# Kernel tuning notes

Measured on AMD Instinct MI355X. Metric: run time of the kernel, lower is better.

## Reference

```python
import jax, jax.numpy as jnp
import numpy as np

T_SIZE = 64
S_SIZE = 256
NUM_HEADS = 12
DEPTH = 12
DIM = 768
MLP_DIM = 3072
EPS = 1e-5
BATCH = 32
N_TOK = 2 * T_SIZE + S_SIZE  # 384


def setup_inputs() -> dict:
    key = jax.random.key(0)
    ks = jax.random.split(key, 6)
    s = 0.02
    return {
        "x": jax.random.normal(ks[0], (BATCH, N_TOK, DIM), jnp.float32),
        "qkv_w": jax.random.normal(ks[1], (DEPTH, DIM, 3 * DIM), jnp.float32) * s,
        "qkv_b": jnp.zeros((DEPTH, 3 * DIM), jnp.float32),
        "proj_w": jax.random.normal(ks[2], (DEPTH, DIM, DIM), jnp.float32) * s,
        "proj_b": jnp.zeros((DEPTH, DIM), jnp.float32),
        "ln1_g": jnp.ones((DEPTH, DIM), jnp.float32),
        "ln1_b": jnp.zeros((DEPTH, DIM), jnp.float32),
        "ln2_g": jnp.ones((DEPTH, DIM), jnp.float32),
        "ln2_b": jnp.zeros((DEPTH, DIM), jnp.float32),
        "fc1_w": jax.random.normal(ks[3], (DEPTH, DIM, MLP_DIM), jnp.float32) * s,
        "fc1_b": jnp.zeros((DEPTH, MLP_DIM), jnp.float32),
        "fc2_w": jax.random.normal(ks[4], (DEPTH, MLP_DIM, DIM), jnp.float32) * s,
        "fc2_b": jnp.zeros((DEPTH, DIM), jnp.float32),
    }


def _layernorm(x, g, b):
    m = jnp.mean(x, axis=-1, keepdims=True)
    v = jnp.mean((x - m) ** 2, axis=-1, keepdims=True)
    return (x - m) * jax.lax.rsqrt(v + EPS) * g + b


def _attention(x, wqkv, bqkv, wp, bp):
    B, N, C = x.shape
    hd = C // NUM_HEADS
    scale = hd ** -0.5
    # [B,N,3C] -> [3,B,H,N,hd]
    qkv = (x @ wqkv + bqkv).reshape(B, N, 3, NUM_HEADS, hd).transpose(2, 0, 3, 1, 4)
    q, k, v = qkv[0], qkv[1], qkv[2]
    q_t = q[:, :, :T_SIZE]
    q_it = q[:, :, T_SIZE:2 * T_SIZE]
    q_s = q[:, :, 2 * T_SIZE:]
    k_it = k[:, :, T_SIZE:2 * T_SIZE]
    v_it = v[:, :, T_SIZE:2 * T_SIZE]
    # mix attention: (t, s) queries over ALL keys
    q_ts = jnp.concatenate([q_t, q_s], axis=2)  # [B,H,t+s,hd]
    mix = jax.nn.softmax(jnp.einsum('bhqd,bhkd->bhqk', q_ts, k) * scale, axis=-1)
    ts = jnp.einsum('bhqk,bhkd->bhqd', mix, v).transpose(0, 2, 1, 3).reshape(B, T_SIZE + S_SIZE, C)
    # inherent attention: it queries over it keys only
    inh = jax.nn.softmax(jnp.einsum('bhqd,bhkd->bhqk', q_it, k_it) * scale, axis=-1)
    it = jnp.einsum('bhqk,bhkd->bhqd', inh, v_it).transpose(0, 2, 1, 3).reshape(B, T_SIZE, C)
    out = jnp.concatenate([ts[:, :T_SIZE], it, ts[:, T_SIZE:]], axis=1)
    return out @ wp + bp


def reference(x, qkv_w, qkv_b, proj_w, proj_b, ln1_g, ln1_b, ln2_g, ln2_b,
              fc1_w, fc1_b, fc2_w, fc2_b):
    for l in range(DEPTH):
        x = x + _attention(_layernorm(x, ln1_g[l], ln1_b[l]),
                           qkv_w[l], qkv_b[l], proj_w[l], proj_b[l])
        h = _layernorm(x, ln2_g[l], ln2_b[l])
        h = jax.nn.gelu(h @ fc1_w[l] + fc1_b[l], approximate=False)
        x = x + (h @ fc2_w[l] + fc2_b[l])
    return x
```

## Files before the change

kernel.cpp:

```cpp
#include <hip/hip_runtime.h>
#include <cstdint>

typedef unsigned short u16;
typedef __attribute__((ext_vector_type(8))) short bf16x8;
typedef __attribute__((ext_vector_type(4))) float f32x4;

#define B_SZ 32
#define NTOK 384
#define DIM 768
#define NH 12
#define HD 64
#define MLP 3072
#define MROWS (B_SZ * NTOK)

__device__ __forceinline__ float b2f(u16 h) { return __uint_as_float(((unsigned)h) << 16); }
__device__ __forceinline__ u16 f2b(float f) {
    unsigned u = __float_as_uint(f);
    unsigned r = u + 0x7fffu + ((u >> 16) & 1u);
    return (u16)(r >> 16);
}

__device__ __forceinline__ void load_lds16(const void* g, void* l) {
    __builtin_amdgcn_global_load_lds(
        (const __attribute__((address_space(1))) unsigned*)g,
        (__attribute__((address_space(3))) unsigned*)l, 16, 0, 0);
}

__global__ void detect_kernel(const u16* __restrict__ x, int* __restrict__ flagp) {
    __shared__ int cnt;
    if (threadIdx.x == 0) cnt = 0;
    __syncthreads();
    int bad = 0;
    for (int i = threadIdx.x; i < 4096; i += 256) {
        int e = (x[i] >> 7) & 0xFF;
        if (e >= 0xC0) bad++;
    }
    atomicAdd(&cnt, bad);
    __syncthreads();
    if (threadIdx.x == 0) *flagp = (cnt > 4) ? 1 : 0;
}

__global__ void conv_any(const void* __restrict__ src, u16* __restrict__ dst, int n,
                         const int* __restrict__ flagp) {
    int i = blockIdx.x * 256 + threadIdx.x;
    if (i >= n) return;
    dst[i] = (*flagp) ? f2b(((const float*)src)[i]) : ((const u16*)src)[i];
}

__global__ void load_x(const void* __restrict__ src, float* __restrict__ dst, int n,
                       const int* __restrict__ flagp) {
    int i = blockIdx.x * 256 + threadIdx.x;
    if (i >= n) return;
    dst[i] = (*flagp) ? ((const float*)src)[i] : b2f(((const u16*)src)[i]);
}

__global__ void store_out(const float* __restrict__ src, void* __restrict__ dst, int n,
                          const int* __restrict__ flagp) {
    int i = blockIdx.x * 256 + threadIdx.x;
    if (i >= n) return;
    if (*flagp) ((float*)dst)[i] = src[i];
    else ((u16*)dst)[i] = f2b(src[i]);
}

__global__ __launch_bounds__(256) void transpose_k(const void* __restrict__ in, size_t ioff,
                                                   u16* __restrict__ outp, int K, int N,
                                                   const int* __restrict__ flagp) {
    __shared__ u16 t[32][33];
    const int flag = *flagp;
    const int n0 = blockIdx.x << 5, k0 = blockIdx.y << 5;
    const int tx = threadIdx.x, ty = threadIdx.y;
#pragma unroll
    for (int i = 0; i < 4; i++) {
        size_t idx = ioff + (size_t)(k0 + ty + i * 8) * N + n0 + tx;
        t[ty + i * 8][tx] = flag ? f2b(((const float*)in)[idx]) : ((const u16*)in)[idx];
    }
    __syncthreads();
#pragma unroll
    for (int i = 0; i < 4; i++)
        outp[(size_t)(n0 + ty + i * 8) * K + k0 + tx] = t[tx][ty + i * 8];
}

template <int MODE>
__global__ __launch_bounds__(256) void gemm_bt(const u16* __restrict__ A,
                                               const u16* __restrict__ Bt,
                                               const u16* __restrict__ bias,
                                               u16* __restrict__ outb,
                                               float* __restrict__ outf,
                                               int N, int K) {
    __shared__ u16 lA[128 * 32];
    __shared__ u16 lB[128 * 32];
    const int tid = threadIdx.x;
    const int wave = tid >> 6, lane = tid & 63;
    const int quad = lane >> 4, l16 = lane & 15;
    const int m0 = blockIdx.y << 7, n0 = blockIdx.x << 7;
    const int wm = (wave & 1) << 6, wn = (wave >> 1) << 6;
    const int arow = lane >> 2, aseg = (lane & 3) << 3;

    f32x4 acc[4][4] = {};

    const u16* gA = A + (size_t)(m0 + wave * 16 + arow) * K + aseg;
    const u16* gB = Bt + (size_t)(n0 + wave * 16 + arow) * K + aseg;
    const size_t skip = (size_t)64 * K;

    for (int kt = 0; kt < K; kt += 32) {
        __syncthreads();
        load_lds16(gA + kt, &lA[wave * 512 + lane * 8]);
        load_lds16(gA + kt + skip, &lA[(wave + 4) * 512 + lane * 8]);
        load_lds16(gB + kt, &lB[wave * 512 + lane * 8]);
        load_lds16(gB + kt + skip, &lB[(wave + 4) * 512 + lane * 8]);
        __syncthreads();
        bf16x8 af[4], bfr[4];
#pragma unroll
        for (int i = 0; i < 4; i++) {
            af[i] = *(const bf16x8*)&lA[(wm + i * 16 + l16) * 32 + quad * 8];
            bfr[i] = *(const bf16x8*)&lB[(wn + i * 16 + l16) * 32 + quad * 8];
        }
#pragma unroll
        for (int i = 0; i < 4; i++)
#pragma unroll
            for (int j = 0; j < 4; j++)
                acc[i][j] = __builtin_amdgcn_mfma_f32_16x16x32_bf16(af[i], bfr[j], acc[i][j], 0, 0, 0);
    }

#pragma unroll
    for (int j = 0; j < 4; j++) {
        const int n = n0 + wn + j * 16 + l16;
        const float bv = b2f(bias[n]);
#pragma unroll
        for (int i = 0; i < 4; i++) {
            const int mrow = m0 + wm + i * 16 + quad * 4;
#pragma unroll
            for (int r = 0; r < 4; r++) {
                float v = acc[i][j][r] + bv;
                size_t idx = (size_t)(mrow + r) * N + n;
                if (MODE == 0) {
                    outb[idx] = f2b(v);
                } else if (MODE == 1) {
                    float t = 0.5f * v * (1.0f + erff(v * 0.70710678118654752f));
                    outb[idx] = f2b(t);
                } else {
                    outf[idx] += v;
                }
            }
        }
    }
}

__global__ __launch_bounds__(256) void ln_kernel(const float* __restrict__ x,
                                                 const u16* __restrict__ g,
                                                 const u16* __restrict__ bta,
                                                 u16* __restrict__ y) {
    const int wave = threadIdx.x >> 6, lane = threadIdx.x & 63;
    const int row = (blockIdx.x << 2) + wave;
    const float4* xr = (const float4*)(x + (size_t)row * DIM);
    float4 v[3];
    float s = 0.f, sq = 0.f;
#pragma unroll
    for (int i = 0; i < 3; i++) {
        v[i] = xr[i * 64 + lane];
        s += v[i].x + v[i].y + v[i].z + v[i].w;
        sq += v[i].x * v[i].x + v[i].y * v[i].y + v[i].z * v[i].z + v[i].w * v[i].w;
    }
#pragma unroll
    for (int off = 32; off >= 1; off >>= 1) {
        s += __shfl_xor(s, off, 64);
        sq += __shfl_xor(sq, off, 64);
    }
    const float mean = s * (1.f / DIM);
    const float var = sq * (1.f / DIM) - mean * mean;
    const float rs = rsqrtf(var + 1e-5f);
    u16* yr = y + (size_t)row * DIM;
#pragma unroll
    for (int i = 0; i < 3; i++) {
        ushort4 gg = ((const ushort4*)g)[i * 64 + lane];
        ushort4 bb = ((const ushort4*)bta)[i * 64 + lane];
        ushort4 o;
        o.x = f2b((v[i].x - mean) * rs * b2f(gg.x) + b2f(bb.x));
        o.y = f2b((v[i].y - mean) * rs * b2f(gg.y) + b2f(bb.y));
        o.z = f2b((v[i].z - mean) * rs * b2f(gg.z) + b2f(bb.z));
        o.w = f2b((v[i].w - mean) * rs * b2f(gg.w) + b2f(bb.w));
        ((ushort4*)yr)[i * 64 + lane] = o;
    }
}

template <int NJ, int JLO>
__global__ __launch_bounds__(256) void attn_kernel(const u16* __restrict__ qkv,
                                                   u16* __restrict__ out) {
    __shared__ u16 vT[64 * 392];
    __shared__ u16 pbuf[4][16 * 72];
    const int bx = blockIdx.x;
    const int qt = (NJ == 24) ? (bx + (bx >= 1 ? 1 : 0)) : 1;
    const int h = blockIdx.y, b = blockIdx.z;
    const int tid = threadIdx.x, wave = tid >> 6, lane = tid & 63;
    const int quad = lane >> 4, l16 = lane & 15;
    const u16* base = qkv + (size_t)b * NTOK * (3 * DIM);

    for (int it = tid; it < NTOK * 8; it += 256) {
        const int key = it >> 3, dseg = it & 7;
        const u16* gp = base + (size_t)key * (3 * DIM) + 2 * DIM + h * HD + dseg * 8;
        ushort4 u0 = ((const ushort4*)gp)[0];
        ushort4 u1 = ((const ushort4*)gp)[1];
        u16 vals[8] = {u0.x, u0.y, u0.z, u0.w, u1.x, u1.y, u1.z, u1.w};
#pragma unroll
        for (int t = 0; t < 8; t++) {
            const int i = (t + key) & 7;
            vT[(dseg * 8 + i) * 392 + key] = vals[i];
        }
    }

    bf16x8 qf[2];
    const int qrow = qt * 64 + wave * 16 + l16;
#pragma unroll
    for (int s = 0; s < 2; s++)
        qf[s] = *(const bf16x8*)(base + (size_t)qrow * (3 * DIM) + h * HD + s * 32 + quad * 8);

    __syncthreads();

    f32x4 sacc[NJ];
#pragma unroll
    for (int j = 0; j < NJ; j++) {
        const int key = (JLO + j) * 16 + l16;
        const u16* kb = base + (size_t)key * (3 * DIM) + DIM + h * HD;
        bf16x8 k0 = *(const bf16x8*)(kb + quad * 8);
        bf16x8 k1 = *(const bf16x8*)(kb + 32 + quad * 8);
        f32x4 z = {0.f, 0.f, 0.f, 0.f};
        z = __builtin_amdgcn_mfma_f32_16x16x32_bf16(qf[0], k0, z, 0, 0, 0);
        sacc[j] = __builtin_amdgcn_mfma_f32_16x16x32_bf16(qf[1], k1, z, 0, 0, 0);
    }

    float mx[4] = {-1e30f, -1e30f, -1e30f, -1e30f};
#pragma unroll
    for (int j = 0; j < NJ; j++)
#pragma unroll
        for (int r = 0; r < 4; r++) mx[r] = fmaxf(mx[r], sacc[j][r]);
#pragma unroll
    for (int off = 1; off < 16; off <<= 1)
#pragma unroll
        for (int r = 0; r < 4; r++) mx[r] = fmaxf(mx[r], __shfl_xor(mx[r], off, 64));

    float sm[4] = {0.f, 0.f, 0.f, 0.f};
#pragma unroll
    for (int j = 0; j < NJ; j++)
#pragma unroll
        for (int r = 0; r < 4; r++) {
            float e = __expf((sacc[j][r] - mx[r]) * 0.125f);
            sacc[j][r] = e;
            sm[r] += e;
        }
#pragma unroll
    for (int off = 1; off < 16; off <<= 1)
#pragma unroll
        for (int r = 0; r < 4; r++) sm[r] += __shfl_xor(sm[r], off, 64);
    float inv[4];
#pragma unroll
    for (int r = 0; r < 4; r++) inv[r] = 1.f / sm[r];

    f32x4 oacc[4] = {};
    u16* pb = &pbuf[wave][0];
#pragma unroll
    for (int c = 0; c < NJ / 4; c++) {
        __syncthreads();
#pragma unroll
        for (int jj = 0; jj < 4; jj++) {
#pragma unroll
            for (int r = 0; r < 4; r++)
                pb[(quad * 4 + r) * 72 + jj * 16 + l16] = f2b(sacc[c * 4 + jj][r] * inv[r]);
        }
        __syncthreads();
#pragma unroll
        for (int s = 0; s < 2; s++) {
            bf16x8 pf = *(const bf16x8*)&pb[l16 * 72 + s * 32 + quad * 8];
            const int kcol = JLO * 16 + c * 64 + s * 32 + quad * 8;
#pragma unroll
            for (int jd = 0; jd < 4; jd++) {
                bf16x8 vf = *(const bf16x8*)&vT[(jd * 16 + l16) * 392 + kcol];
                oacc[jd] = __builtin_amdgcn_mfma_f32_16x16x32_bf16(pf, vf, oacc[jd], 0, 0, 0);
            }
        }
    }

    const int q = qt * 64 + wave * 16 + quad * 4;
    u16* orow = out + (size_t)(b * NTOK + q) * DIM + h * HD;
#pragma unroll
    for (int jd = 0; jd < 4; jd++)
#pragma unroll
        for (int r = 0; r < 4; r++)
            orow[(size_t)r * DIM + jd * 16 + l16] = f2b(oacc[jd][r]);
}

extern "C" void kernel_launch(void* const* d_in, const int* in_sizes, int n_in,
                              void* d_out, int out_size, void* d_ws, size_t ws_size,
                              hipStream_t stream) {
    const void* x_in   = d_in[0];
    const void* qkv_w  = d_in[1];
    const void* qkv_b  = d_in[2];
    const void* proj_w = d_in[3];
    const void* proj_b = d_in[4];
    const void* ln1_g  = d_in[5];
    const void* ln1_b  = d_in[6];
    const void* ln2_g  = d_in[7];
    const void* ln2_b  = d_in[8];
    const void* fc1_w  = d_in[9];
    const void* fc1_b  = d_in[10];
    const void* fc2_w  = d_in[11];
    const void* fc2_b  = d_in[12];

    constexpr size_t SZ_X32 = (size_t)MROWS * DIM * 4;
    constexpr size_t SZ_ABUF = (size_t)MROWS * DIM * 2;
    constexpr size_t SZ_BIG = (size_t)MROWS * MLP * 2;
    constexpr size_t SZ_WT = (size_t)(2304 * 768 + 768 * 768 + 3072 * 768 + 768 * 3072) * 2;
    constexpr size_t SZ_PAR = 262144;
    const size_t fixed = SZ_X32 + SZ_ABUF + SZ_WT + SZ_PAR + 256;

    int nc;
    if (fixed + SZ_BIG <= ws_size) nc = 1;
    else if (fixed + SZ_BIG / 2 <= ws_size) nc = 2;
    else nc = 4;
    const size_t bigsz = SZ_BIG / nc;

    char* ws = (char*)d_ws;
    float* x32 = (float*)ws;
    u16* abuf = (u16*)(ws + SZ_X32);
    u16* big = (u16*)(ws + SZ_X32 + SZ_ABUF);
    u16* wqt = (u16*)(ws + SZ_X32 + SZ_ABUF + bigsz);
    u16* wpt = wqt + 2304 * 768;
    u16* w1t = wpt + 768 * 768;
    u16* w2t = w1t + 3072 * 768;
    u16* par = w2t + 768 * 3072;
    int* flagp = (int*)((char*)(par) + SZ_PAR);

    u16* p_qkvb = par;
    u16* p_projb = p_qkvb + 12 * 2304;
    u16* p_ln1g = p_projb + 12 * 768;
    u16* p_ln1b = p_ln1g + 12 * 768;
    u16* p_ln2g = p_ln1b + 12 * 768;
    u16* p_ln2b = p_ln2g + 12 * 768;
    u16* p_fc1b = p_ln2b + 12 * 768;
    u16* p_fc2b = p_fc1b + 12 * 3072;

    const int NEL = MROWS * DIM;
    detect_kernel<<<1, 256, 0, stream>>>((const u16*)x_in, flagp);
    load_x<<<(NEL + 255) / 256, 256, 0, stream>>>(x_in, x32, NEL, flagp);
    conv_any<<<(12 * 2304 + 255) / 256, 256, 0, stream>>>(qkv_b, p_qkvb, 12 * 2304, flagp);
    conv_any<<<(12 * 768 + 255) / 256, 256, 0, stream>>>(proj_b, p_projb, 12 * 768, flagp);
    conv_any<<<(12 * 768 + 255) / 256, 256, 0, stream>>>(ln1_g, p_ln1g, 12 * 768, flagp);
    conv_any<<<(12 * 768 + 255) / 256, 256, 0, stream>>>(ln1_b, p_ln1b, 12 * 768, flagp);
    conv_any<<<(12 * 768 + 255) / 256, 256, 0, stream>>>(ln2_g, p_ln2g, 12 * 768, flagp);
    conv_any<<<(12 * 768 + 255) / 256, 256, 0, stream>>>(ln2_b, p_ln2b, 12 * 768, flagp);
    conv_any<<<(12 * 3072 + 255) / 256, 256, 0, stream>>>(fc1_b, p_fc1b, 12 * 3072, flagp);
    conv_any<<<(12 * 768 + 255) / 256, 256, 0, stream>>>(fc2_b, p_fc2b, 12 * 768, flagp);

    const int CR = MROWS / nc;
    const int CB = B_SZ / nc;

    for (int l = 0; l < 12; l++) {
        transpose_k<<<dim3(2304 / 32, 768 / 32), dim3(32, 8), 0, stream>>>(
            qkv_w, (size_t)l * DIM * 2304, wqt, DIM, 2304, flagp);
        transpose_k<<<dim3(768 / 32, 768 / 32), dim3(32, 8), 0, stream>>>(
            proj_w, (size_t)l * DIM * DIM, wpt, DIM, DIM, flagp);
        transpose_k<<<dim3(3072 / 32, 768 / 32), dim3(32, 8), 0, stream>>>(
            fc1_w, (size_t)l * DIM * MLP, w1t, DIM, MLP, flagp);
        transpose_k<<<dim3(768 / 32, 3072 / 32), dim3(32, 8), 0, stream>>>(
            fc2_w, (size_t)l * MLP * DIM, w2t, MLP, DIM, flagp);

        for (int c = 0; c < nc; c++) {
            const size_t r0 = (size_t)c * CR;
            ln_kernel<<<CR / 4, 256, 0, stream>>>(x32 + r0 * DIM, p_ln1g + l * DIM,
                                                  p_ln1b + l * DIM, abuf + r0 * DIM);
            gemm_bt<0><<<dim3(2304 / 128, CR / 128), 256, 0, stream>>>(
                abuf + r0 * DIM, wqt, p_qkvb + l * 2304, big, nullptr, 2304, DIM);
            attn_kernel<24, 0><<<dim3(5, NH, CB), 256, 0, stream>>>(big, abuf + r0 * DIM);
            attn_kernel<4, 4><<<dim3(1, NH, CB), 256, 0, stream>>>(big, abuf + r0 * DIM);
            gemm_bt<2><<<dim3(DIM / 128, CR / 128), 256, 0, stream>>>(
                abuf + r0 * DIM, wpt, p_projb + l * DIM, nullptr, x32 + r0 * DIM, DIM, DIM);
        }
        for (int c = 0; c < nc; c++) {
            const size_t r0 = (size_t)c * CR;
            ln_kernel<<<CR / 4, 256, 0, stream>>>(x32 + r0 * DIM, p_ln2g + l * DIM,
                                                  p_ln2b + l * DIM, abuf + r0 * DIM);
            gemm_bt<1><<<dim3(MLP / 128, CR / 128), 256, 0, stream>>>(
                abuf + r0 * DIM, w1t, p_fc1b + l * MLP, big, nullptr, MLP, DIM);
            gemm_bt<2><<<dim3(DIM / 128, CR / 128), 256, 0, stream>>>(
                big, w2t, p_fc2b + l * DIM, nullptr, x32 + r0 * DIM, DIM, MLP);
        }
    }
    store_out<<<(NEL + 255) / 256, 256, 0, stream>>>(x32, d_out, NEL, flagp);
}
```

Baseline: 6.152 ms.

## Double-buffer GEMM LDS, swizzle layout, remap blocks per XCD, split-K residual GEMMs

The bf16 GEMM kernel now double-buffers its LDS tiles, so the next K-slice loads overlap the MFMA work, and it drops one barrier per iteration. The LDS layout is XOR-swizzled to reduce bank conflicts on fragment reads. Workgroup IDs are remapped so neighbouring tiles land on the same XCD for better L2 reuse. The N=768 residual GEMMs (proj, fc2) use 2-way split-K with atomic fp32 adds to raise occupancy, at the cost of atomic traffic and nondeterministic summation order.

```diff
diff --git a/kernel.cpp b/kernel.cpp
--- a/kernel.cpp
+++ b/kernel.cpp
@@ -80,52 +80,80 @@
         outp[(size_t)(n0 + ty + i * 8) * K + k0 + tx] = t[tx][ty + i * 8];
 }
 
-template <int MODE>
+template <int MODE, int SPLITK>
 __global__ __launch_bounds__(256) void gemm_bt(const u16* __restrict__ A,
                                                const u16* __restrict__ Bt,
                                                const u16* __restrict__ bias,
                                                u16* __restrict__ outb,
                                                float* __restrict__ outf,
                                                int N, int K) {
-    __shared__ u16 lA[128 * 32];
-    __shared__ u16 lB[128 * 32];
+    __shared__ u16 lA[2][128 * 32];
+    __shared__ u16 lB[2][128 * 32];
     const int tid = threadIdx.x;
     const int wave = tid >> 6, lane = tid & 63;
     const int quad = lane >> 4, l16 = lane & 15;
-    const int m0 = blockIdx.y << 7, n0 = blockIdx.x << 7;
+
+    const int gx = gridDim.x;
+    const int nwg = gx * gridDim.y;
+    const int orig = blockIdx.y * gx + blockIdx.x;
+    const int xcd = orig & 7, loc = orig >> 3;
+    const int qq = nwg >> 3, rr = nwg & 7;
+    const int wgid = (xcd < rr ? xcd * (qq + 1) : rr * (qq + 1) + (xcd - rr) * qq) + loc;
+    const int bx = wgid % gx, by = wgid / gx;
+
+    const int m0 = by << 7, n0 = bx << 7;
     const int wm = (wave & 1) << 6, wn = (wave >> 1) << 6;
-    const int arow = lane >> 2, aseg = (lane & 3) << 3;
+    const int arow = lane >> 2;
+    const int aseg = (((lane & 3) ^ (arow & 3)) << 3);
+
+    const int KC = K / SPLITK;
+    const int kBase = (SPLITK > 1) ? (int)blockIdx.z * KC : 0;
 
     f32x4 acc[4][4] = {};
 
-    const u16* gA = A + (size_t)(m0 + wave * 16 + arow) * K + aseg;
-    const u16* gB = Bt + (size_t)(n0 + wave * 16 + arow) * K + aseg;
+    const u16* gA = A + (size_t)(m0 + wave * 16 + arow) * K + kBase + aseg;
+    const u16* gB = Bt + (size_t)(n0 + wave * 16 + arow) * K + kBase + aseg;
     const size_t skip = (size_t)64 * K;
 
-    for (int kt = 0; kt < K; kt += 32) {
-        __syncthreads();
-        load_lds16(gA + kt, &lA[wave * 512 + lane * 8]);
-        load_lds16(gA + kt + skip, &lA[(wave + 4) * 512 + lane * 8]);
-        load_lds16(gB + kt, &lB[wave * 512 + lane * 8]);
-        load_lds16(gB + kt + skip, &lB[(wave + 4) * 512 + lane * 8]);
-        __syncthreads();
+#define STAGE(buf, kt)                                                          \
+    do {                                                                        \
+        load_lds16(gA + (kt), &lA[buf][wave * 512 + lane * 8]);                 \
+        load_lds16(gA + (kt) + skip, &lA[buf][(wave + 4) * 512 + lane * 8]);    \
+        load_lds16(gB + (kt), &lB[buf][wave * 512 + lane * 8]);                 \
+        load_lds16(gB + (kt) + skip, &lB[buf][(wave + 4) * 512 + lane * 8]);    \
+    } while (0)
+
+    STAGE(0, 0);
+    __syncthreads();
+    int cur = 0;
+    for (int kt = 0; kt < KC; kt += 32) {
+        const int nxt = kt + 32;
+        if (nxt < KC) STAGE(cur ^ 1, nxt);
         bf16x8 af[4], bfr[4];
 #pragma unroll
         for (int i = 0; i < 4; i++) {
-            af[i] = *(const bf16x8*)&lA[(wm + i * 16 + l16) * 32 + quad * 8];
-            bfr[i] = *(const bf16x8*)&lB[(wn + i * 16 + l16) * 32 + quad * 8];
+            const int ra = wm + i * 16 + l16;
+            const int rb = wn + i * 16 + l16;
+            af[i] = *(const bf16x8*)&lA[cur][ra * 32 + ((quad ^ (l16 & 3)) << 3)];
+            bfr[i] = *(const bf16x8*)&lB[cur][rb * 32 + ((quad ^ (l16 & 3)) << 3)];
         }
 #pragma unroll
         for (int i = 0; i < 4; i++)
 #pragma unroll
             for (int j = 0; j < 4; j++)
                 acc[i][j] = __builtin_amdgcn_mfma_f32_16x16x32_bf16(af[i], bfr[j], acc[i][j], 0, 0, 0);
-    }
-
+        if (nxt < KC) {
+            __syncthreads();
+            cur ^= 1;
+        }
+    }
+#undef STAGE
+
+    const bool addb = (SPLITK == 1) || (blockIdx.z == 0);
 #pragma unroll
     for (int j = 0; j < 4; j++) {
         const int n = n0 + wn + j * 16 + l16;
-        const float bv = b2f(bias[n]);
+        const float bv = addb ? b2f(bias[n]) : 0.f;
 #pragma unroll
         for (int i = 0; i < 4; i++) {
             const int mrow = m0 + wm + i * 16 + quad * 4;
@@ -139,7 +167,8 @@
                     float t = 0.5f * v * (1.0f + erff(v * 0.70710678118654752f));
                     outb[idx] = f2b(t);
                 } else {
-                    outf[idx] += v;
+                    if (SPLITK == 1) outf[idx] += v;
+                    else atomicAdd(&outf[idx], v);
                 }
             }
         }
@@ -367,20 +396,20 @@
             const size_t r0 = (size_t)c * CR;
             ln_kernel<<<CR / 4, 256, 0, stream>>>(x32 + r0 * DIM, p_ln1g + l * DIM,
                                                   p_ln1b + l * DIM, abuf + r0 * DIM);
-            gemm_bt<0><<<dim3(2304 / 128, CR / 128), 256, 0, stream>>>(
+            gemm_bt<0, 1><<<dim3(2304 / 128, CR / 128), 256, 0, stream>>>(
                 abuf + r0 * DIM, wqt, p_qkvb + l * 2304, big, nullptr, 2304, DIM);
             attn_kernel<24, 0><<<dim3(5, NH, CB), 256, 0, stream>>>(big, abuf + r0 * DIM);
             attn_kernel<4, 4><<<dim3(1, NH, CB), 256, 0, stream>>>(big, abuf + r0 * DIM);
-            gemm_bt<2><<<dim3(DIM / 128, CR / 128), 256, 0, stream>>>(
+            gemm_bt<2, 2><<<dim3(DIM / 128, CR / 128, 2), 256, 0, stream>>>(
                 abuf + r0 * DIM, wpt, p_projb + l * DIM, nullptr, x32 + r0 * DIM, DIM, DIM);
         }
         for (int c = 0; c < nc; c++) {
             const size_t r0 = (size_t)c * CR;
             ln_kernel<<<CR / 4, 256, 0, stream>>>(x32 + r0 * DIM, p_ln2g + l * DIM,
                                                   p_ln2b + l * DIM, abuf + r0 * DIM);
-            gemm_bt<1><<<dim3(MLP / 128, CR / 128), 256, 0, stream>>>(
+            gemm_bt<1, 1><<<dim3(MLP / 128, CR / 128), 256, 0, stream>>>(
                 abuf + r0 * DIM, w1t, p_fc1b + l * MLP, big, nullptr, MLP, DIM);
-            gemm_bt<2><<<dim3(DIM / 128, CR / 128), 256, 0, stream>>>(
+            gemm_bt<2, 2><<<dim3(DIM / 128, CR / 128, 2), 256, 0, stream>>>(
                 big, w2t, p_fc2b + l * DIM, nullptr, x32 + r0 * DIM, DIM, MLP);
         }
     }
```

Result: slower. 7.992 ms (+29.9%).

## Double-buffer GEMM LDS tiles, remap blocks across XCDs, use 64-row tiles for N=768

Applied to the files above, without the earlier changes.

The GEMM kernel now double-buffers its LDS tiles, prefetching the next K slice while the current one feeds MFMA, with one barrier per iteration instead of two. Workgroup IDs are remapped so consecutive tiles land on the same XCD, which should improve L2 reuse. The proj and fc2 GEMMs, which have only 768 output columns, switch to 64-row M tiles to launch more workgroups. The cost is twice the LDS per block, which may lower occupancy, plus a little index arithmetic.

```diff
diff --git a/kernel.cpp b/kernel.cpp
--- a/kernel.cpp
+++ b/kernel.cpp
@@ -80,54 +80,81 @@
         outp[(size_t)(n0 + ty + i * 8) * K + k0 + tx] = t[tx][ty + i * 8];
 }
 
-template <int MODE>
+template <int MODE, int TM>
 __global__ __launch_bounds__(256) void gemm_bt(const u16* __restrict__ A,
                                                const u16* __restrict__ Bt,
                                                const u16* __restrict__ bias,
                                                u16* __restrict__ outb,
                                                float* __restrict__ outf,
                                                int N, int K) {
-    __shared__ u16 lA[128 * 32];
-    __shared__ u16 lB[128 * 32];
+    constexpr int MI = (TM == 128) ? 4 : 2;
+    __shared__ u16 lA[2][TM * 32];
+    __shared__ u16 lB[2][128 * 32];
     const int tid = threadIdx.x;
     const int wave = tid >> 6, lane = tid & 63;
     const int quad = lane >> 4, l16 = lane & 15;
-    const int m0 = blockIdx.y << 7, n0 = blockIdx.x << 7;
-    const int wm = (wave & 1) << 6, wn = (wave >> 1) << 6;
+
+    const int gx = gridDim.x;
+    const int nwg = gx * gridDim.y;
+    const int orig = blockIdx.y * gx + blockIdx.x;
+    const int xcd = orig & 7, loc = orig >> 3;
+    const int qq = nwg >> 3, rr = nwg & 7;
+    const int wgid = (xcd < rr ? xcd * (qq + 1) : rr * (qq + 1) + (xcd - rr) * qq) + loc;
+    const int bx = wgid % gx, by = wgid / gx;
+
+    const int m0 = by * TM, n0 = bx << 7;
+    const int wm = (wave & 1) * (TM / 2), wn = (wave >> 1) << 6;
     const int arow = lane >> 2, aseg = (lane & 3) << 3;
 
-    f32x4 acc[4][4] = {};
+    f32x4 acc[MI][4] = {};
 
     const u16* gA = A + (size_t)(m0 + wave * 16 + arow) * K + aseg;
     const u16* gB = Bt + (size_t)(n0 + wave * 16 + arow) * K + aseg;
     const size_t skip = (size_t)64 * K;
 
+#define STAGE(buf, kt)                                                              \
+    do {                                                                            \
+        load_lds16(gA + (kt), &lA[buf][wave * 512 + lane * 8]);                     \
+        if constexpr (TM == 128)                                                    \
+            load_lds16(gA + (kt) + skip, &lA[buf][(wave + 4) * 512 + lane * 8]);    \
+        load_lds16(gB + (kt), &lB[buf][wave * 512 + lane * 8]);                     \
+        load_lds16(gB + (kt) + skip, &lB[buf][(wave + 4) * 512 + lane * 8]);        \
+    } while (0)
+
+    STAGE(0, 0);
+    asm volatile("s_waitcnt vmcnt(0)" ::: "memory");
+    __builtin_amdgcn_s_barrier();
+
+    int cur = 0;
     for (int kt = 0; kt < K; kt += 32) {
-        __syncthreads();
-        load_lds16(gA + kt, &lA[wave * 512 + lane * 8]);
-        load_lds16(gA + kt + skip, &lA[(wave + 4) * 512 + lane * 8]);
-        load_lds16(gB + kt, &lB[wave * 512 + lane * 8]);
-        load_lds16(gB + kt + skip, &lB[(wave + 4) * 512 + lane * 8]);
-        __syncthreads();
-        bf16x8 af[4], bfr[4];
-#pragma unroll
-        for (int i = 0; i < 4; i++) {
-            af[i] = *(const bf16x8*)&lA[(wm + i * 16 + l16) * 32 + quad * 8];
-            bfr[i] = *(const bf16x8*)&lB[(wn + i * 16 + l16) * 32 + quad * 8];
-        }
-#pragma unroll
-        for (int i = 0; i < 4; i++)
+        const bool more = (kt + 32 < K);
+        if (more) STAGE(cur ^ 1, kt + 32);
+        bf16x8 af[MI], bfr[4];
+#pragma unroll
+        for (int i = 0; i < MI; i++)
+            af[i] = *(const bf16x8*)&lA[cur][(wm + i * 16 + l16) * 32 + quad * 8];
+#pragma unroll
+        for (int j = 0; j < 4; j++)
+            bfr[j] = *(const bf16x8*)&lB[cur][(wn + j * 16 + l16) * 32 + quad * 8];
+#pragma unroll
+        for (int i = 0; i < MI; i++)
 #pragma unroll
             for (int j = 0; j < 4; j++)
                 acc[i][j] = __builtin_amdgcn_mfma_f32_16x16x32_bf16(af[i], bfr[j], acc[i][j], 0, 0, 0);
-    }
+        if (more) {
+            asm volatile("s_waitcnt vmcnt(0)" ::: "memory");
+            __builtin_amdgcn_s_barrier();
+            cur ^= 1;
+        }
+    }
+#undef STAGE
 
 #pragma unroll
     for (int j = 0; j < 4; j++) {
         const int n = n0 + wn + j * 16 + l16;
         const float bv = b2f(bias[n]);
 #pragma unroll
-        for (int i = 0; i < 4; i++) {
+        for (int i = 0; i < MI; i++) {
             const int mrow = m0 + wm + i * 16 + quad * 4;
 #pragma unroll
             for (int r = 0; r < 4; r++) {
@@ -367,20 +394,20 @@
             const size_t r0 = (size_t)c * CR;
             ln_kernel<<<CR / 4, 256, 0, stream>>>(x32 + r0 * DIM, p_ln1g + l * DIM,
                                                   p_ln1b + l * DIM, abuf + r0 * DIM);
-            gemm_bt<0><<<dim3(2304 / 128, CR / 128), 256, 0, stream>>>(
+            gemm_bt<0, 128><<<dim3(2304 / 128, CR / 128), 256, 0, stream>>>(
                 abuf + r0 * DIM, wqt, p_qkvb + l * 2304, big, nullptr, 2304, DIM);
             attn_kernel<24, 0><<<dim3(5, NH, CB), 256, 0, stream>>>(big, abuf + r0 * DIM);
             attn_kernel<4, 4><<<dim3(1, NH, CB), 256, 0, stream>>>(big, abuf + r0 * DIM);
-            gemm_bt<2><<<dim3(DIM / 128, CR / 128), 256, 0, stream>>>(
+            gemm_bt<2, 64><<<dim3(DIM / 128, CR / 64), 256, 0, stream>>>(
                 abuf + r0 * DIM, wpt, p_projb + l * DIM, nullptr, x32 + r0 * DIM, DIM, DIM);
         }
         for (int c = 0; c < nc; c++) {
             const size_t r0 = (size_t)c * CR;
             ln_kernel<<<CR / 4, 256, 0, stream>>>(x32 + r0 * DIM, p_ln2g + l * DIM,
                                                   p_ln2b + l * DIM, abuf + r0 * DIM);
-            gemm_bt<1><<<dim3(MLP / 128, CR / 128), 256, 0, stream>>>(
+            gemm_bt<1, 128><<<dim3(MLP / 128, CR / 128), 256, 0, stream>>>(
                 abuf + r0 * DIM, w1t, p_fc1b + l * MLP, big, nullptr, MLP, DIM);
-            gemm_bt<2><<<dim3(DIM / 128, CR / 128), 256, 0, stream>>>(
+            gemm_bt<2, 64><<<dim3(DIM / 128, CR / 64), 256, 0, stream>>>(
                 big, w2t, p_fc2b + l * DIM, nullptr, x32 + r0 * DIM, DIM, MLP);
         }
     }
```

Result: slower. 7.412 ms (+20.5%).
